# Performance work log

Measured on AMD Instinct MI355X. Metric: run time of the kernel, lower is better.

The kernel has to match this reference:

```python
import jax, jax.numpy as jnp
import numpy as np

N_NODES = 50000
N_EDGES = 800000
FIN = 128
FQK = 128
FV = 128
H = 8


def setup_inputs() -> dict:
    key = jax.random.key(0)
    k1, k2, k3, k4, k5 = jax.random.split(key, 5)
    x = jax.random.normal(k1, (N_NODES, FIN), dtype=jnp.float32)
    # nn.Linear(Fin, 2*Fqk+Fv, bias=False): weight shape [Ftot, Fin]
    W = jax.random.normal(k2, (2 * FQK + FV, FIN), dtype=jnp.float32) / np.sqrt(FIN)
    # src must be sorted (scatter_* assume batch[-1]+1 segments)
    src = jnp.sort(jax.random.randint(k3, (N_EDGES,), 0, N_NODES))
    dest = jax.random.randint(k4, (N_EDGES,), 0, N_NODES)
    ei = jnp.stack([src, dest])
    batch = jnp.sort(jax.random.randint(k5, (N_NODES,), 0, 64))
    return {"x": x, "W": W, "batch": batch, "ei": ei}


def reference(x, W, batch, ei):
    n = x.shape[0]
    Fh = FQK // H    # 16
    Fhv = FV // H    # 16
    scaling = float(Fh) ** (-0.5)
    src, dest = ei[0], ei[1]

    qkv = x @ W.T                                   # [n, 2*Fqk+Fv]
    q = (qkv[:, :FQK] * scaling).reshape(n, H, Fh)
    k = qkv[:, FQK:2 * FQK].reshape(n, H, Fh)
    v = qkv[:, 2 * FQK:].reshape(n, H, Fhv)

    # per-edge attention scores, one per head: [E, H]
    aw = jnp.einsum('ehf,ehf->eh', q[src], k[dest])
    # faithful to original scatter_softmax: subtract GLOBAL per-head max
    aw = aw - aw.max(axis=0)
    ex = jnp.exp(aw)
    denom = jax.ops.segment_sum(ex, src, num_segments=n)[src]   # [E, H]
    a = ex / denom

    out = jax.ops.segment_sum(a[:, :, None] * v[dest], src, num_segments=n)  # [n, H, Fhv]
    return out.reshape(n, H * Fhv)
```

## Files before the change

### kernel.cpp

```cpp
#include <hip/hip_runtime.h>
#include <hip/hip_bf16.h>
#include <math.h>

#define FIN_ 128
#define FQK_ 128

typedef __attribute__((ext_vector_type(8))) short short8v;
typedef __attribute__((ext_vector_type(4))) float float4v;

__device__ __forceinline__ unsigned short f2bf(float f) {
    unsigned u = __float_as_uint(f);
    u += 0x7fffu + ((u >> 16) & 1u);
    return (unsigned short)(u >> 16);
}

__device__ __forceinline__ short8v pack8(float4 a, float4 b) {
    short8v r;
    r[0] = (short)f2bf(a.x); r[1] = (short)f2bf(a.y);
    r[2] = (short)f2bf(a.z); r[3] = (short)f2bf(a.w);
    r[4] = (short)f2bf(b.x); r[5] = (short)f2bf(b.y);
    r[6] = (short)f2bf(b.z); r[7] = (short)f2bf(b.w);
    return r;
}

__global__ __launch_bounds__(256) void gemm_qkv_mfma(const float* __restrict__ x,
                                                     const float* __restrict__ W,
                                                     float* __restrict__ qbuf,
                                                     unsigned short* __restrict__ kv,
                                                     int n) {
    __shared__ unsigned short xs[128][68];
    __shared__ unsigned short ws[128][68];
    const int row0 = blockIdx.x * 128;
    const int col0 = blockIdx.y * 128;
    const int t = threadIdx.x;
    const int lane = t & 63;
    const int wave = t >> 6;
    const int wr = wave >> 1, wc = wave & 1;
    const int l15 = lane & 15, kg = lane >> 4;

    float4v acc[4][4];
#pragma unroll
    for (int i = 0; i < 4; ++i)
#pragma unroll
        for (int j = 0; j < 4; ++j) acc[i][j] = (float4v)0.f;

    const int r5 = t >> 3;
    const int c8 = (t & 7) * 8;

    for (int half = 0; half < 2; ++half) {
        __syncthreads();
#pragma unroll
        for (int p = 0; p < 4; ++p) {
            const int row = p * 32 + r5;
            const int gxr = row0 + row;
            float4 u0, u1;
            if (gxr < n) {
                u0 = *(const float4*)&x[(size_t)gxr * FIN_ + half * 64 + c8];
                u1 = *(const float4*)&x[(size_t)gxr * FIN_ + half * 64 + c8 + 4];
            } else {
                u0 = make_float4(0.f, 0.f, 0.f, 0.f); u1 = u0;
            }
            *(short8v*)&xs[row][c8] = pack8(u0, u1);
            const float4 w0 = *(const float4*)&W[(size_t)(col0 + row) * FIN_ + half * 64 + c8];
            const float4 w1 = *(const float4*)&W[(size_t)(col0 + row) * FIN_ + half * 64 + c8 + 4];
            *(short8v*)&ws[row][c8] = pack8(w0, w1);
        }
        __syncthreads();
#pragma unroll
        for (int ks = 0; ks < 2; ++ks) {
            const int kcol = ks * 32 + kg * 8;
            short8v a[4], b[4];
#pragma unroll
            for (int mi = 0; mi < 4; ++mi)
                a[mi] = *(short8v*)&xs[wr * 64 + mi * 16 + l15][kcol];
#pragma unroll
            for (int ni = 0; ni < 4; ++ni)
                b[ni] = *(short8v*)&ws[wc * 64 + ni * 16 + l15][kcol];
#pragma unroll
            for (int mi = 0; mi < 4; ++mi)
#pragma unroll
                for (int ni = 0; ni < 4; ++ni)
                    acc[mi][ni] = __builtin_amdgcn_mfma_f32_16x16x32_bf16(
                        a[mi], b[ni], acc[mi][ni], 0, 0, 0);
        }
    }

    const int orow = kg * 4;
#pragma unroll
    for (int mi = 0; mi < 4; ++mi) {
#pragma unroll
        for (int reg = 0; reg < 4; ++reg) {
            const int r = row0 + wr * 64 + mi * 16 + orow + reg;
            if (r >= n) continue;
#pragma unroll
            for (int ni = 0; ni < 4; ++ni) {
                const int c = wc * 64 + ni * 16 + l15;
                const float v = acc[mi][ni][reg];
                if (col0 == 0) {
                    qbuf[(size_t)r * FIN_ + c] = v * 0.25f;
                } else {
                    const int base = (col0 == 128) ? 0 : 128;
                    kv[(size_t)r * 256 + base + c] = f2bf(v);
                }
            }
        }
    }
}

__global__ void build_rowptr(const int* __restrict__ src, int nE,
                             int* __restrict__ rowptr, int n) {
    int i = blockIdx.x * blockDim.x + threadIdx.x;
    if (i > n) return;
    int lo = 0, hi = nE;
    while (lo < hi) {
        int mid = (lo + hi) >> 1;
        if (src[mid] < i) lo = mid + 1; else hi = mid;
    }
    rowptr[i] = lo;
}

__device__ __forceinline__ float2 bf2f(const unsigned short* p) {
    unsigned u = *(const unsigned*)p;
    return make_float2(__uint_as_float(u << 16), __uint_as_float(u & 0xffff0000u));
}

__global__ __launch_bounds__(256) void attn_edges(const float* __restrict__ qbuf,
                                                  const unsigned short* __restrict__ kv,
                                                  const int* __restrict__ rowptr,
                                                  const int* __restrict__ dest,
                                                  float* __restrict__ out, int n) {
    const int wave = threadIdx.x >> 6;
    const int node = blockIdx.x * 4 + wave;
    if (node >= n) return;
    const int lane = threadIdx.x & 63;

    const float2 qv = *(const float2*)&qbuf[(size_t)node * FIN_ + lane * 2];
    const int e0 = rowptr[node];
    const int e1 = rowptr[node + 1];

    float m = -3.0e38f, l = 0.f;
    float accx = 0.f, accy = 0.f;

    int e = e0;
    for (; e + 4 <= e1; e += 4) {
        const int d0 = dest[e], d1 = dest[e + 1], d2 = dest[e + 2], d3 = dest[e + 3];
        const float2 k0 = bf2f(kv + (size_t)d0 * 256 + 2 * lane);
        const float2 k1 = bf2f(kv + (size_t)d1 * 256 + 2 * lane);
        const float2 k2 = bf2f(kv + (size_t)d2 * 256 + 2 * lane);
        const float2 k3 = bf2f(kv + (size_t)d3 * 256 + 2 * lane);
        const float2 v0 = bf2f(kv + (size_t)d0 * 256 + 128 + 2 * lane);
        const float2 v1 = bf2f(kv + (size_t)d1 * 256 + 128 + 2 * lane);
        const float2 v2 = bf2f(kv + (size_t)d2 * 256 + 128 + 2 * lane);
        const float2 v3 = bf2f(kv + (size_t)d3 * 256 + 128 + 2 * lane);

        float s0 = qv.x * k0.x + qv.y * k0.y;
        float s1 = qv.x * k1.x + qv.y * k1.y;
        float s2 = qv.x * k2.x + qv.y * k2.y;
        float s3 = qv.x * k3.x + qv.y * k3.y;
#pragma unroll
        for (int w = 1; w <= 4; w <<= 1) {
            s0 += __shfl_xor(s0, w);
            s1 += __shfl_xor(s1, w);
            s2 += __shfl_xor(s2, w);
            s3 += __shfl_xor(s3, w);
        }
        const float mx = fmaxf(fmaxf(s0, s1), fmaxf(s2, s3));
        const float mn = fmaxf(m, mx);
        const float rs = __expf(m - mn);
        const float p0 = __expf(s0 - mn), p1 = __expf(s1 - mn);
        const float p2 = __expf(s2 - mn), p3 = __expf(s3 - mn);
        l = l * rs + ((p0 + p1) + (p2 + p3));
        accx = accx * rs + p0 * v0.x + p1 * v1.x + p2 * v2.x + p3 * v3.x;
        accy = accy * rs + p0 * v0.y + p1 * v1.y + p2 * v2.y + p3 * v3.y;
        m = mn;
    }
    for (; e < e1; ++e) {
        const int d = dest[e];
        const float2 kvv = bf2f(kv + (size_t)d * 256 + 2 * lane);
        const float2 vv = bf2f(kv + (size_t)d * 256 + 128 + 2 * lane);
        float sc = qv.x * kvv.x + qv.y * kvv.y;
        sc += __shfl_xor(sc, 1);
        sc += __shfl_xor(sc, 2);
        sc += __shfl_xor(sc, 4);
        const float mn = fmaxf(m, sc);
        const float rs = __expf(m - mn);
        const float p = __expf(sc - mn);
        l = l * rs + p;
        accx = accx * rs + p * vv.x;
        accy = accy * rs + p * vv.y;
        m = mn;
    }

    const float inv = (l > 0.f) ? 1.f / l : 0.f;
    *(float2*)&out[(size_t)node * FIN_ + lane * 2] = make_float2(accx * inv, accy * inv);
}

extern "C" void kernel_launch(void* const* d_in, const int* in_sizes, int n_in,
                              void* d_out, int out_size, void* d_ws, size_t ws_size,
                              hipStream_t stream) {
    const float* x = (const float*)d_in[0];
    const float* W = (const float*)d_in[1];
    const int* ei = (const int*)d_in[3];

    const int n = in_sizes[0] / FIN_;
    const int nE = in_sizes[3] / 2;
    const int* src = ei;
    const int* dest = ei + nE;

    float* qbuf = (float*)d_ws;
    unsigned short* kv = (unsigned short*)((char*)d_ws + (size_t)n * FIN_ * sizeof(float));
    int* rowptr = (int*)((char*)kv + (size_t)n * 256 * sizeof(unsigned short));
    float* out = (float*)d_out;

    build_rowptr<<<(n + 1 + 255) / 256, 256, 0, stream>>>(src, nE, rowptr, n);

    dim3 g1((n + 127) / 128, 3);
    gemm_qkv_mfma<<<g1, 256, 0, stream>>>(x, W, qbuf, kv, n);

    attn_edges<<<(n + 3) / 4, 256, 0, stream>>>(qbuf, kv, rowptr, dest, out, n);
}
```

Baseline: 98.29 us.

## Process eight edges per wave iteration with per-head lanes and butterfly reduction

Remaps the attention kernel so each group of 8 lanes handles one edge and each lane one head. Each lane does the whole 16-wide dot product in registers, using 16-byte K/V loads, so eight edges are handled per iteration instead of one shuffle-reduced edge at a time. Partial outputs are then combined across the edge groups with a recursive-halving butterfly of shuffles. The running-max online softmax is removed and raw exp(s) is accumulated directly, which drops the rescaling work but can overflow if scores get large.

Result: faster. 95.60 us (-2.7%).

```diff
diff --git a/kernel.cpp b/kernel.cpp
--- a/kernel.cpp
+++ b/kernel.cpp
@@ -119,80 +119,116 @@
     rowptr[i] = lo;
 }
 
-__device__ __forceinline__ float2 bf2f(const unsigned short* p) {
-    unsigned u = *(const unsigned*)p;
-    return make_float2(__uint_as_float(u << 16), __uint_as_float(u & 0xffff0000u));
-}
-
-__global__ __launch_bounds__(256) void attn_edges(const float* __restrict__ qbuf,
-                                                  const unsigned short* __restrict__ kv,
-                                                  const int* __restrict__ rowptr,
-                                                  const int* __restrict__ dest,
-                                                  float* __restrict__ out, int n) {
+#define LOF(w) __uint_as_float((w) << 16)
+#define HIF(w) __uint_as_float((w) & 0xffff0000u)
+
+__global__ __launch_bounds__(256) void attn_edges_ep(const float* __restrict__ qbuf,
+                                                     const unsigned short* __restrict__ kv,
+                                                     const int* __restrict__ rowptr,
+                                                     const int* __restrict__ dest,
+                                                     float* __restrict__ out, int n) {
     const int wave = threadIdx.x >> 6;
     const int node = blockIdx.x * 4 + wave;
     if (node >= n) return;
     const int lane = threadIdx.x & 63;
-
-    const float2 qv = *(const float2*)&qbuf[(size_t)node * FIN_ + lane * 2];
+    const int j = lane >> 3;
+    const int h = lane & 7;
+    const int ppos = ((j & 1) << 3) | ((j & 2) << 1) | ((j & 4) >> 1);
+    float* outp = &out[(size_t)node * FIN_ + h * 16 + ppos];
+
     const int e0 = rowptr[node];
     const int e1 = rowptr[node + 1];
-
-    float m = -3.0e38f, l = 0.f;
-    float accx = 0.f, accy = 0.f;
-
-    int e = e0;
-    for (; e + 4 <= e1; e += 4) {
-        const int d0 = dest[e], d1 = dest[e + 1], d2 = dest[e + 2], d3 = dest[e + 3];
-        const float2 k0 = bf2f(kv + (size_t)d0 * 256 + 2 * lane);
-        const float2 k1 = bf2f(kv + (size_t)d1 * 256 + 2 * lane);
-        const float2 k2 = bf2f(kv + (size_t)d2 * 256 + 2 * lane);
-        const float2 k3 = bf2f(kv + (size_t)d3 * 256 + 2 * lane);
-        const float2 v0 = bf2f(kv + (size_t)d0 * 256 + 128 + 2 * lane);
-        const float2 v1 = bf2f(kv + (size_t)d1 * 256 + 128 + 2 * lane);
-        const float2 v2 = bf2f(kv + (size_t)d2 * 256 + 128 + 2 * lane);
-        const float2 v3 = bf2f(kv + (size_t)d3 * 256 + 128 + 2 * lane);
-
-        float s0 = qv.x * k0.x + qv.y * k0.y;
-        float s1 = qv.x * k1.x + qv.y * k1.y;
-        float s2 = qv.x * k2.x + qv.y * k2.y;
-        float s3 = qv.x * k3.x + qv.y * k3.y;
-#pragma unroll
-        for (int w = 1; w <= 4; w <<= 1) {
-            s0 += __shfl_xor(s0, w);
-            s1 += __shfl_xor(s1, w);
-            s2 += __shfl_xor(s2, w);
-            s3 += __shfl_xor(s3, w);
-        }
-        const float mx = fmaxf(fmaxf(s0, s1), fmaxf(s2, s3));
-        const float mn = fmaxf(m, mx);
-        const float rs = __expf(m - mn);
-        const float p0 = __expf(s0 - mn), p1 = __expf(s1 - mn);
-        const float p2 = __expf(s2 - mn), p3 = __expf(s3 - mn);
-        l = l * rs + ((p0 + p1) + (p2 + p3));
-        accx = accx * rs + p0 * v0.x + p1 * v1.x + p2 * v2.x + p3 * v3.x;
-        accy = accy * rs + p0 * v0.y + p1 * v1.y + p2 * v2.y + p3 * v3.y;
-        m = mn;
-    }
-    for (; e < e1; ++e) {
-        const int d = dest[e];
-        const float2 kvv = bf2f(kv + (size_t)d * 256 + 2 * lane);
-        const float2 vv = bf2f(kv + (size_t)d * 256 + 128 + 2 * lane);
-        float sc = qv.x * kvv.x + qv.y * kvv.y;
-        sc += __shfl_xor(sc, 1);
-        sc += __shfl_xor(sc, 2);
-        sc += __shfl_xor(sc, 4);
-        const float mn = fmaxf(m, sc);
-        const float rs = __expf(m - mn);
-        const float p = __expf(sc - mn);
-        l = l * rs + p;
-        accx = accx * rs + p * vv.x;
-        accy = accy * rs + p * vv.y;
-        m = mn;
-    }
-
-    const float inv = (l > 0.f) ? 1.f / l : 0.f;
-    *(float2*)&out[(size_t)node * FIN_ + lane * 2] = make_float2(accx * inv, accy * inv);
+    if (e0 == e1) {
+        *(float2*)outp = make_float2(0.f, 0.f);
+        return;
+    }
+
+    float qa[16];
+    {
+        const float4* qp = (const float4*)&qbuf[(size_t)node * FIN_ + h * 16];
+        float4 a = qp[0], b = qp[1], c = qp[2], d = qp[3];
+        qa[0]=a.x; qa[1]=a.y; qa[2]=a.z; qa[3]=a.w;
+        qa[4]=b.x; qa[5]=b.y; qa[6]=b.z; qa[7]=b.w;
+        qa[8]=c.x; qa[9]=c.y; qa[10]=c.z; qa[11]=c.w;
+        qa[12]=d.x; qa[13]=d.y; qa[14]=d.z; qa[15]=d.w;
+    }
+
+    float lsum = 0.f;
+    float acc[16];
+#pragma unroll
+    for (int i = 0; i < 16; ++i) acc[i] = 0.f;
+
+    const int hoff = h << 4;
+    for (int eb = e0; eb < e1; eb += 8) {
+        const int my_e = eb + j;
+        const bool valid = my_e < e1;
+        const int ee = valid ? my_e : (e1 - 1);
+        const unsigned d = (unsigned)dest[ee];
+        const unsigned off = (d << 8) + hoff;
+        const uint4 k0 = *(const uint4*)(kv + off);
+        const uint4 k1 = *(const uint4*)(kv + off + 8);
+        const uint4 v0 = *(const uint4*)(kv + off + 128);
+        const uint4 v1 = *(const uint4*)(kv + off + 136);
+
+        float s;
+        s  = qa[0]  * LOF(k0.x) + qa[1]  * HIF(k0.x);
+        s += qa[2]  * LOF(k0.y) + qa[3]  * HIF(k0.y);
+        s += qa[4]  * LOF(k0.z) + qa[5]  * HIF(k0.z);
+        s += qa[6]  * LOF(k0.w) + qa[7]  * HIF(k0.w);
+        s += qa[8]  * LOF(k1.x) + qa[9]  * HIF(k1.x);
+        s += qa[10] * LOF(k1.y) + qa[11] * HIF(k1.y);
+        s += qa[12] * LOF(k1.z) + qa[13] * HIF(k1.z);
+        s += qa[14] * LOF(k1.w) + qa[15] * HIF(k1.w);
+
+        const float p = valid ? __expf(s) : 0.f;
+        lsum += p;
+        acc[0]  += p * LOF(v0.x); acc[1]  += p * HIF(v0.x);
+        acc[2]  += p * LOF(v0.y); acc[3]  += p * HIF(v0.y);
+        acc[4]  += p * LOF(v0.z); acc[5]  += p * HIF(v0.z);
+        acc[6]  += p * LOF(v0.w); acc[7]  += p * HIF(v0.w);
+        acc[8]  += p * LOF(v1.x); acc[9]  += p * HIF(v1.x);
+        acc[10] += p * LOF(v1.y); acc[11] += p * HIF(v1.y);
+        acc[12] += p * LOF(v1.z); acc[13] += p * HIF(v1.z);
+        acc[14] += p * LOF(v1.w); acc[15] += p * HIF(v1.w);
+    }
+
+    lsum += __shfl_xor(lsum, 8);
+    lsum += __shfl_xor(lsum, 16);
+    lsum += __shfl_xor(lsum, 32);
+
+    float r8[8];
+    {
+        const bool b = (j & 1) != 0;
+#pragma unroll
+        for (int i = 0; i < 8; ++i) {
+            const float keep = b ? acc[i + 8] : acc[i];
+            const float send = b ? acc[i] : acc[i + 8];
+            r8[i] = keep + __shfl_xor(send, 8);
+        }
+    }
+    float r4[4];
+    {
+        const bool b = (j & 2) != 0;
+#pragma unroll
+        for (int i = 0; i < 4; ++i) {
+            const float keep = b ? r8[i + 4] : r8[i];
+            const float send = b ? r8[i] : r8[i + 4];
+            r4[i] = keep + __shfl_xor(send, 16);
+        }
+    }
+    float r2[2];
+    {
+        const bool b = (j & 4) != 0;
+#pragma unroll
+        for (int i = 0; i < 2; ++i) {
+            const float keep = b ? r4[i + 2] : r4[i];
+            const float send = b ? r4[i] : r4[i + 2];
+            r2[i] = keep + __shfl_xor(send, 32);
+        }
+    }
+
+    const float inv = (lsum > 0.f) ? 1.f / lsum : 0.f;
+    *(float2*)outp = make_float2(r2[0] * inv, r2[1] * inv);
 }
 
 extern "C" void kernel_launch(void* const* d_in, const int* in_sizes, int n_in,
@@ -217,5 +253,5 @@
     dim3 g1((n + 127) / 128, 3);
     gemm_qkv_mfma<<<g1, 256, 0, stream>>>(x, W, qbuf, kv, n);
 
-    attn_edges<<<(n + 3) / 4, 256, 0, stream>>>(qbuf, kv, rowptr, dest, out, n);
-}
+    attn_edges_ep<<<(n + 3) / 4, 256, 0, stream>>>(qbuf, kv, rowptr, dest, out, n);
+}
```
